# Optimization experiments

Hardware: AMD Instinct MI355X
Metric: run time of the kernel (lower is better)

The kernel has to match this reference:

```python
import jax, jax.numpy as jnp
import numpy as np
from jax import lax

KH, KW, PAD = 3, 3, 1  # kernel_size and paddings from init_kwargs


def _sign_pm1(v):
    # tf.sign with zeros mapped to -1
    return jnp.where(v > 0, jnp.float32(1.0), jnp.float32(-1.0)).astype(v.dtype)


def setup_inputs() -> dict:
    key = jax.random.key(0)
    k1, k2, k3 = jax.random.split(key, 3)
    x = jax.random.normal(k1, (32, 56, 56, 256), dtype=jnp.float32)
    kernel = jax.random.normal(k2, (KH, KW, 256, 256), dtype=jnp.float32) * 0.05
    bias = jax.random.normal(k3, (256,), dtype=jnp.float32) * 0.01
    return {"x": x, "kernel": kernel, "bias": bias}


def reference(x, kernel, bias):
    # pad input spatially (NHWC)
    xp = jnp.pad(x, ((0, 0), (PAD, PAD), (PAD, PAD), (0, 0)))

    # binarize kernel: static batch dim known -> alpha = mean(|W|) over (kh, kw, cin)
    bin_k = _sign_pm1(kernel)
    alpha = jnp.mean(jnp.abs(kernel), axis=(0, 1, 2))  # (Cout,)

    # binarize input: batch dim dynamic in TF -> beta = mean(|x|) over channels, keepdims
    bin_x = _sign_pm1(xp)                               # (N, H+2P, W+2P, C)
    beta = jnp.mean(jnp.abs(xp), axis=3, keepdims=True)  # (N, H+2P, W+2P, 1)

    # K = avg_pool(beta, kernel window, stride 1, VALID)
    K = lax.reduce_window(beta, jnp.float32(0.0), lax.add,
                          (1, KH, KW, 1), (1, 1, 1, 1), 'VALID') / (KH * KW)
    Ka = K * alpha  # (N, H, W, Cout) via broadcast

    conv = lax.conv_general_dilated(
        bin_x, bin_k, window_strides=(1, 1), padding='VALID',
        dimension_numbers=('NHWC', 'HWIO', 'NHWC'))  # (N, H, W, Cout)

    return conv * Ka + bias
```

## Files before the change

kernel.cpp:

```cpp
#include <hip/hip_runtime.h>
#include <cstdint>
#include <cstddef>

#define N_ 32
#define H_ 56
#define W_ 56
#define C_ 256
#define HP 58
#define WP 58

typedef int v4i  __attribute__((ext_vector_type(4)));
typedef int v16i __attribute__((ext_vector_type(16)));

__global__ __launch_bounds__(256) void pack_w(const float* __restrict__ k,
                                              signed char* __restrict__ wi8,
                                              float* __restrict__ palpha) {
    int idx = blockIdx.x;
    int p = idx >> 2, q = idx & 3;
    int co = threadIdx.x;
    float s = 0.f;
    #pragma unroll
    for (int half = 0; half < 2; ++half) {
        int kc = q * 2 + half;
        unsigned wrd[8];
        #pragma unroll
        for (int e = 0; e < 8; ++e) {
            unsigned wv = 0;
            #pragma unroll
            for (int j = 0; j < 4; ++j) {
                float v = k[(size_t)(p * 256 + kc * 32 + e * 4 + j) * 256 + co];
                s += fabsf(v);
                wv |= ((v > 0.f) ? 0x01u : 0xFFu) << (8 * j);
            }
            wrd[e] = wv;
        }
        v4i lo = {(int)wrd[0], (int)wrd[1], (int)wrd[2], (int)wrd[3]};
        v4i hi = {(int)wrd[4], (int)wrd[5], (int)wrd[6], (int)wrd[7]};
        size_t base = ((size_t)(p * 8 + kc) * 256 + co) * 2;
        ((v4i*)wi8)[base]     = lo;
        ((v4i*)wi8)[base + 1] = hi;
    }
    palpha[idx * 256 + co] = s;
}

__device__ __forceinline__ void epilogue(const v16i& acc, int mb, int svar,
                                         const float* bS, float alpha, float bv,
                                         int co, size_t obase,
                                         float* __restrict__ out) {
    #pragma unroll
    for (int r = 0; r < 16; ++r) {
        int row = (r & 3) + 8 * (r >> 2) + 4 * svar;
        int m = mb + row;
        if (m < 112) {
            int hl = (m >= 56);
            int w = m - 56 * hl;
            float val = (float)acc[r] * (bS[m] * alpha) + bv;
            out[obase + ((size_t)hl * W_ + w) * C_ + co] = val;
        }
    }
}

__global__ __launch_bounds__(512, 4) void bconv(
        const float4* __restrict__ x4,
        const signed char* __restrict__ wi8, const float* __restrict__ palpha,
        const float* __restrict__ bias, float* __restrict__ out) {
    int bid = blockIdx.x;
    int bi = (bid & 7) * 112 + (bid >> 3);
    int n = bi / 28;
    int hb = (bi - n * 28) * 2;

    int tid = threadIdx.x;
    int lane = tid & 63, wid = tid >> 6;
    int wm = wid >> 2, wn = wid & 3;
    int l31 = lane & 31, svar = lane >> 5;

    __shared__ __align__(16) signed char xs[4 * WP * 256];
    __shared__ float brow[4 * WP];
    __shared__ float bS[112];

    {
        int sl4 = lane >> 2;
        int bo  = (lane & 3) << 2;
        for (int i = 0; i < 29; ++i) {
            int pp = wid + 8 * i;
            int r = pp / WP, xc = pp - r * WP;
            int ypad = hb + r;
            bool inb = (ypad >= 1 && ypad <= H_ && xc >= 1 && xc <= W_);
            float4 v = make_float4(0.f, 0.f, 0.f, 0.f);
            if (inb)
                v = x4[(((size_t)n * H_ + (ypad - 1)) * W_ + (xc - 1)) * 64 + lane];
            unsigned wb = ((v.x > 0.f) ? 0x01u : 0xFFu)
                        | (((v.y > 0.f) ? 0x01u : 0xFFu) << 8)
                        | (((v.z > 0.f) ? 0x01u : 0xFFu) << 16)
                        | (((v.w > 0.f) ? 0x01u : 0xFFu) << 24);
            *(unsigned*)&xs[pp * 256 + ((sl4 ^ (pp & 15)) << 4) + bo] = wb;
            float s = fabsf(v.x) + fabsf(v.y) + fabsf(v.z) + fabsf(v.w);
            #pragma unroll
            for (int m = 32; m >= 1; m >>= 1) s += __shfl_xor(s, m, 64);
            if (lane == 0) brow[pp] = s * (1.f / 256.f);
        }
    }
    __syncthreads();

    if (tid < 112) {
        int r = (tid >= 56);
        int w = tid - 56 * r;
        float s = 0.f;
        #pragma unroll
        for (int rr = 0; rr < 3; ++rr)
            #pragma unroll
            for (int d = 0; d < 3; ++d) s += brow[(r + rr) * WP + w + d];
        bS[tid] = s * (1.f / 9.f);
    }

    int m0 = wm * 64 + l31;
    int m1 = m0 + 32;
    int m1e = m1 < 112 ? m1 : 111;
    int hl0 = (m0 >= 56), hl1 = (m1e >= 56);
    int pb0 = hl0 * WP + (m0 - 56 * hl0);
    int pb1 = hl1 * WP + (m1e - 56 * hl1);

    int co0 = wn * 64 + l31, co1 = co0 + 32;
    int vb0 = co0 * 2 + svar, vb1 = vb0 + 64;

    v16i acc00 = {0,0,0,0,0,0,0,0,0,0,0,0,0,0,0,0};
    v16i acc01 = acc00, acc10 = acc00, acc11 = acc00;

    const v4i* xsv = (const v4i*)xs;
    const v4i* wv  = (const v4i*)wi8;

    int a0c = pb0 << 4, x0c = pb0 & 15;
    int a1c = pb1 << 4, x1c = pb1 & 15;
    const v4i* bqc = wv;

    v4i A0 = xsv[a0c | (svar ^ x0c)];
    v4i A1 = xsv[a1c | (svar ^ x1c)];
    v4i B0 = bqc[vb0];
    v4i B1 = bqc[vb1];

    for (int tap = 0; tap < 9; ++tap) {
        int tn = (tap < 8) ? tap + 1 : 8;
        int khn = (tn * 11) >> 5, kwn = tn - khn * 3;
        int p0n = pb0 + khn * WP + kwn, p1n = pb1 + khn * WP + kwn;
        int a0n = p0n << 4, x0n = p0n & 15;
        int a1n = p1n << 4, x1n = p1n & 15;
        const v4i* bqn = wv + (size_t)tn * 4096;
        #pragma unroll
        for (int kc = 0; kc < 8; ++kc) {
            const int nkc = (kc == 7) ? 0 : kc + 1;
            const int sln = nkc * 2 + svar;
            int A0a, A1a;
            const v4i* bq2;
            if (kc == 7) { A0a = a0n | (sln ^ x0n); A1a = a1n | (sln ^ x1n); bq2 = bqn; }
            else         { A0a = a0c | (sln ^ x0c); A1a = a1c | (sln ^ x1c); bq2 = bqc; }
            v4i A0n_ = xsv[A0a];
            v4i A1n_ = xsv[A1a];
            v4i B0n_ = bq2[nkc * 512 + vb0];
            v4i B1n_ = bq2[nkc * 512 + vb1];
            acc00 = __builtin_amdgcn_mfma_i32_32x32x32_i8(A0, B0, acc00, 0, 0, 0);
            acc01 = __builtin_amdgcn_mfma_i32_32x32x32_i8(A0, B1, acc01, 0, 0, 0);
            acc10 = __builtin_amdgcn_mfma_i32_32x32x32_i8(A1, B0, acc10, 0, 0, 0);
            acc11 = __builtin_amdgcn_mfma_i32_32x32x32_i8(A1, B1, acc11, 0, 0, 0);
            A0 = A0n_; A1 = A1n_; B0 = B0n_; B1 = B1n_;
        }
        a0c = a0n; x0c = x0n; a1c = a1n; x1c = x1n; bqc = bqn;
    }

    __syncthreads();

    float a0s = 0.f, a1s = 0.f;
    for (int i = 0; i < 36; ++i) {
        a0s += palpha[i * 256 + co0];
        a1s += palpha[i * 256 + co1];
    }
    a0s *= (1.f / 2304.f);
    a1s *= (1.f / 2304.f);
    float bv0 = bias[co0], bv1 = bias[co1];

    size_t obase = (size_t)(n * H_ + hb) * W_ * C_;
    epilogue(acc00, wm * 64,      svar, bS, a0s, bv0, co0, obase, out);
    epilogue(acc01, wm * 64,      svar, bS, a1s, bv1, co1, obase, out);
    epilogue(acc10, wm * 64 + 32, svar, bS, a0s, bv0, co0, obase, out);
    epilogue(acc11, wm * 64 + 32, svar, bS, a1s, bv1, co1, obase, out);
}

extern "C" void kernel_launch(void* const* d_in, const int* in_sizes, int n_in,
                              void* d_out, int out_size, void* d_ws, size_t ws_size,
                              hipStream_t stream) {
    const float* x    = (const float*)d_in[0];
    const float* k    = (const float*)d_in[1];
    const float* bias = (const float*)d_in[2];
    float* out = (float*)d_out;

    char* ws = (char*)d_ws;
    signed char* wi8    = (signed char*)(ws);
    float*       palpha = (float*)(ws + 589824);

    pack_w<<<36, 256, 0, stream>>>(k, wi8, palpha);
    bconv<<<896, 512, 0, stream>>>((const float4*)x, wi8, palpha, bias, out);
}
```

Before: 260.0 us.

## Halve block to 4 waves, give each wave a 64x128 output tile

The block shrinks from 8 waves to 4, and each wave now computes 2x4 MFMA tiles (64 rows by 128 output channels) instead of 2x2. This reuses each A fragment across four B fragments, which cuts LDS reads of A per MFMA and the number of waves reloading the same weights. The software-pipelined prefetch of the next A/B fragments is removed in favour of plain loads inside the unrolled loop. The cost is double the accumulator registers per wave (8 v16i), fewer waves to hide global weight-load latency, and a slower input staging phase with half the threads.

```diff
diff --git a/kernel.cpp b/kernel.cpp
--- a/kernel.cpp
+++ b/kernel.cpp
@@ -60,7 +60,7 @@
     }
 }
 
-__global__ __launch_bounds__(512, 4) void bconv(
+__global__ __launch_bounds__(256, 2) void bconv(
         const float4* __restrict__ x4,
         const signed char* __restrict__ wi8, const float* __restrict__ palpha,
         const float* __restrict__ bias, float* __restrict__ out) {
@@ -71,7 +71,7 @@
 
     int tid = threadIdx.x;
     int lane = tid & 63, wid = tid >> 6;
-    int wm = wid >> 2, wn = wid & 3;
+    int wm = wid >> 1, wn = wid & 1;
     int l31 = lane & 31, svar = lane >> 5;
 
     __shared__ __align__(16) signed char xs[4 * WP * 256];
@@ -81,8 +81,8 @@
     {
         int sl4 = lane >> 2;
         int bo  = (lane & 3) << 2;
-        for (int i = 0; i < 29; ++i) {
-            int pp = wid + 8 * i;
+        for (int i = 0; i < 58; ++i) {
+            int pp = wid + 4 * i;
             int r = pp / WP, xc = pp - r * WP;
             int ypad = hb + r;
             bool inb = (ypad >= 1 && ypad <= H_ && xc >= 1 && xc <= W_);
@@ -120,68 +120,65 @@
     int pb0 = hl0 * WP + (m0 - 56 * hl0);
     int pb1 = hl1 * WP + (m1e - 56 * hl1);
 
-    int co0 = wn * 64 + l31, co1 = co0 + 32;
-    int vb0 = co0 * 2 + svar, vb1 = vb0 + 64;
+    int vbb = (wn * 128 + l31) * 2 + svar;
 
-    v16i acc00 = {0,0,0,0,0,0,0,0,0,0,0,0,0,0,0,0};
-    v16i acc01 = acc00, acc10 = acc00, acc11 = acc00;
+    v16i acc0[4], acc1[4];
+    #pragma unroll
+    for (int t = 0; t < 4; ++t) {
+        acc0[t] = (v16i){0,0,0,0,0,0,0,0,0,0,0,0,0,0,0,0};
+        acc1[t] = acc0[t];
+    }
 
     const v4i* xsv = (const v4i*)xs;
     const v4i* wv  = (const v4i*)wi8;
 
-    int a0c = pb0 << 4, x0c = pb0 & 15;
-    int a1c = pb1 << 4, x1c = pb1 & 15;
-    const v4i* bqc = wv;
-
-    v4i A0 = xsv[a0c | (svar ^ x0c)];
-    v4i A1 = xsv[a1c | (svar ^ x1c)];
-    v4i B0 = bqc[vb0];
-    v4i B1 = bqc[vb1];
-
     for (int tap = 0; tap < 9; ++tap) {
-        int tn = (tap < 8) ? tap + 1 : 8;
-        int khn = (tn * 11) >> 5, kwn = tn - khn * 3;
-        int p0n = pb0 + khn * WP + kwn, p1n = pb1 + khn * WP + kwn;
-        int a0n = p0n << 4, x0n = p0n & 15;
-        int a1n = p1n << 4, x1n = p1n & 15;
-        const v4i* bqn = wv + (size_t)tn * 4096;
+        int kh = (tap * 11) >> 5;
+        int kw = tap - kh * 3;
+        int p0 = pb0 + kh * WP + kw;
+        int p1 = pb1 + kh * WP + kw;
+        int a0 = p0 << 4, x0 = p0 & 15;
+        int a1 = p1 << 4, x1 = p1 & 15;
+        const v4i* bq = wv + (size_t)tap * 4096;
         #pragma unroll
         for (int kc = 0; kc < 8; ++kc) {
-            const int nkc = (kc == 7) ? 0 : kc + 1;
-            const int sln = nkc * 2 + svar;
-            int A0a, A1a;
-            const v4i* bq2;
-            if (kc == 7) { A0a = a0n | (sln ^ x0n); A1a = a1n | (sln ^ x1n); bq2 = bqn; }
-            else         { A0a = a0c | (sln ^ x0c); A1a = a1c | (sln ^ x1c); bq2 = bqc; }
-            v4i A0n_ = xsv[A0a];
-            v4i A1n_ = xsv[A1a];
-            v4i B0n_ = bq2[nkc * 512 + vb0];
-            v4i B1n_ = bq2[nkc * 512 + vb1];
-            acc00 = __builtin_amdgcn_mfma_i32_32x32x32_i8(A0, B0, acc00, 0, 0, 0);
-            acc01 = __builtin_amdgcn_mfma_i32_32x32x32_i8(A0, B1, acc01, 0, 0, 0);
-            acc10 = __builtin_amdgcn_mfma_i32_32x32x32_i8(A1, B0, acc10, 0, 0, 0);
-            acc11 = __builtin_amdgcn_mfma_i32_32x32x32_i8(A1, B1, acc11, 0, 0, 0);
-            A0 = A0n_; A1 = A1n_; B0 = B0n_; B1 = B1n_;
+            v4i B0 = bq[kc * 512 + vbb];
+            v4i B1 = bq[kc * 512 + vbb + 64];
+            v4i B2 = bq[kc * 512 + vbb + 128];
+            v4i B3 = bq[kc * 512 + vbb + 192];
+            int sl = kc * 2 + svar;
+            v4i A0 = xsv[a0 | (sl ^ x0)];
+            v4i A1 = xsv[a1 | (sl ^ x1)];
+            acc0[0] = __builtin_amdgcn_mfma_i32_32x32x32_i8(A0, B0, acc0[0], 0, 0, 0);
+            acc1[0] = __builtin_amdgcn_mfma_i32_32x32x32_i8(A1, B0, acc1[0], 0, 0, 0);
+            acc0[1] = __builtin_amdgcn_mfma_i32_32x32x32_i8(A0, B1, acc0[1], 0, 0, 0);
+            acc1[1] = __builtin_amdgcn_mfma_i32_32x32x32_i8(A1, B1, acc1[1], 0, 0, 0);
+            acc0[2] = __builtin_amdgcn_mfma_i32_32x32x32_i8(A0, B2, acc0[2], 0, 0, 0);
+            acc1[2] = __builtin_amdgcn_mfma_i32_32x32x32_i8(A1, B2, acc1[2], 0, 0, 0);
+            acc0[3] = __builtin_amdgcn_mfma_i32_32x32x32_i8(A0, B3, acc0[3], 0, 0, 0);
+            acc1[3] = __builtin_amdgcn_mfma_i32_32x32x32_i8(A1, B3, acc1[3], 0, 0, 0);
         }
-        a0c = a0n; x0c = x0n; a1c = a1n; x1c = x1n; bqc = bqn;
     }
 
     __syncthreads();
 
-    float a0s = 0.f, a1s = 0.f;
-    for (int i = 0; i < 36; ++i) {
-        a0s += palpha[i * 256 + co0];
-        a1s += palpha[i * 256 + co1];
+    float as[4], bvv[4];
+    #pragma unroll
+    for (int t = 0; t < 4; ++t) {
+        int co = wn * 128 + t * 32 + l31;
+        float s = 0.f;
+        for (int i = 0; i < 36; ++i) s += palpha[i * 256 + co];
+        as[t] = s * (1.f / 2304.f);
+        bvv[t] = bias[co];
     }
-    a0s *= (1.f / 2304.f);
-    a1s *= (1.f / 2304.f);
-    float bv0 = bias[co0], bv1 = bias[co1];
 
     size_t obase = (size_t)(n * H_ + hb) * W_ * C_;
-    epilogue(acc00, wm * 64,      svar, bS, a0s, bv0, co0, obase, out);
-    epilogue(acc01, wm * 64,      svar, bS, a1s, bv1, co1, obase, out);
-    epilogue(acc10, wm * 64 + 32, svar, bS, a0s, bv0, co0, obase, out);
-    epilogue(acc11, wm * 64 + 32, svar, bS, a1s, bv1, co1, obase, out);
+    #pragma unroll
+    for (int t = 0; t < 4; ++t) {
+        int co = wn * 128 + t * 32 + l31;
+        epilogue(acc0[t], wm * 64,      svar, bS, as[t], bvv[t], co, obase, out);
+        epilogue(acc1[t], wm * 64 + 32, svar, bS, as[t], bvv[t], co, obase, out);
+    }
 }
 
 extern "C" void kernel_launch(void* const* d_in, const int* in_sizes, int n_in,
@@ -197,5 +194,5 @@
     float*       palpha = (float*)(ws + 589824);
 
     pack_w<<<36, 256, 0, stream>>>(k, wi8, palpha);
-    bconv<<<896, 512, 0, stream>>>((const float4*)x, wi8, palpha, bias, out);
+    bconv<<<896, 256, 0, stream>>>((const float4*)x, wi8, palpha, bias, out);
 }
```

After: 352.7 us. 35.7% more time.
